# Optimization experiments

Hardware: AMD Instinct MI355X
Metric: run time of the kernel (lower is better)

Reference implementation:

```python
import jax, jax.numpy as jnp
import numpy as np

B, N, E, D, L, NC = 64, 128, 1024, 256, 2, 7
BETA = 0.3  # args.diffloss
BIG = 1e30  # mask_logic constant (score - (1-adj)*1e30), as in torch source lineage


def setup_inputs():
    key = jax.random.key(0)
    ks = iter(jax.random.split(key, 48))
    def p(shape, s=0.02):
        return jax.random.normal(next(ks), shape, jnp.float32) * s
    inp = {}
    inp["features"] = jax.random.normal(next(ks), (B, N, E), jnp.float32)
    inp["adj_1"] = jax.random.randint(next(ks), (B, N, N), 0, 2, jnp.int32)
    inp["adj_2"] = jax.random.randint(next(ks), (B, N, N), 0, 2, jnp.int32)
    inp["s_mask"] = jax.random.randint(next(ks), (B, N, N), 0, 2, jnp.int32)
    inp["s_mask_onehot"] = jnp.zeros((B, N, N, 2), jnp.int32)
    inp["lengths"] = jnp.full((B,), N, jnp.int32)
    inp["fc1_w"] = p((D, E)); inp["fc1_b"] = jnp.zeros((D,), jnp.float32)
    # GRUCell params (torch layout: weight_ih (3D,D) order r,z,n)
    for nm in ["gcs", "gps", "gcl", "gpl"]:
        inp[nm + "_wih"] = p((L, 3 * D, D)); inp[nm + "_whh"] = p((L, 3 * D, D))
        inp[nm + "_bih"] = jnp.zeros((L, 3 * D), jnp.float32)
        inp[nm + "_bhh"] = jnp.zeros((L, 3 * D), jnp.float32)
    # GatDot params per layer: linear1 (Q proj), linear2 (K proj)
    for nm in ["gats", "gatl"]:
        inp[nm + "_wq"] = p((L, D, D)); inp[nm + "_bq"] = jnp.zeros((L, D), jnp.float32)
        inp[nm + "_wk"] = p((L, D, D)); inp[nm + "_bk"] = jnp.zeros((L, D), jnp.float32)
    inp["affine1"] = p((2 * D, 2 * D), 0.05)
    inp["affine2"] = p((2 * D, 2 * D), 0.05)
    IN = 4 * D + E  # hidden*2*2 + emb_dim
    inp["mlp_w1"] = p((D, IN)); inp["mlp_b1"] = jnp.zeros((D,), jnp.float32)
    inp["mlp_w2"] = p((D, D)); inp["mlp_b2"] = jnp.zeros((D,), jnp.float32)
    inp["out_w"] = p((NC, D)); inp["out_b"] = jnp.zeros((NC,), jnp.float32)
    return inp


def gru_cell(x, h, wih, whh, bih, bhh):
    gi = x @ wih.T + bih
    gh = h @ whh.T + bhh
    ir, iz, in_ = jnp.split(gi, 3, axis=-1)
    hr, hz, hn = jnp.split(gh, 3, axis=-1)
    r = jax.nn.sigmoid(ir + hr)
    z = jax.nn.sigmoid(iz + hz)
    n = jnp.tanh(in_ + r * hn)
    return (1.0 - z) * n + z * h


def dag_pass(H_in, adj, gat, cpar, ppar):
    """Sequential DAG pass: per-utterance masked dot-product gather + GRU-C/GRU-P."""
    wq, bq, wk, bk = gat
    n = H_in.shape[1]
    idx = jnp.arange(n)

    def step(carry, inp):
        H1, Kb = carry            # H1: [B,N,D] written prefix; Kb = linear2(H1)
        i, x, arow = inp          # x: [B,D], arow: [B,N]
        q = x @ wq.T + bq
        scores = jnp.einsum('bnd,bd->bn', Kb, q)
        # torch: alpha - (1-adj)*1e30 over prefix :i; positions >= i excluded
        logits = scores - (1.0 - arow) * BIG - (idx >= i).astype(scores.dtype) * (2.0 * BIG)
        w = jax.nn.softmax(logits, axis=-1)
        M = jnp.einsum('bn,bnd->bd', w, H1)  # exactly 0 at i==0 (buffer zeros)
        C = gru_cell(x, M, *cpar)   # grus_c(input=x, hidden=M)
        P = gru_cell(M, x, *ppar)   # grus_p(input=M, hidden=x)
        h = C + P
        H1 = jax.lax.dynamic_update_slice(H1, h[:, None, :], (0, i, 0))
        Kb = jax.lax.dynamic_update_slice(Kb, (h @ wk.T + bk)[:, None, :], (0, i, 0))
        return (H1, Kb), None

    init = (jnp.zeros_like(H_in), jnp.zeros_like(H_in))
    xs = (idx, jnp.swapaxes(H_in, 0, 1), jnp.swapaxes(adj, 0, 1))
    (H1, _), _ = jax.lax.scan(step, init, xs)
    return H1


def diff_loss_fn(a, b):
    # orthogonality (DSN-style) loss between short/long channel features
    x = a.reshape(-1, a.shape[-1])
    y = b.reshape(-1, b.shape[-1])
    x = x - x.mean(axis=0, keepdims=True)
    y = y - y.mean(axis=0, keepdims=True)
    x = x / (jnp.linalg.norm(x, axis=1, keepdims=True) + 1e-6)
    y = y / (jnp.linalg.norm(y, axis=1, keepdims=True) + 1e-6)
    return jnp.mean((x.T @ y) ** 2)


def _forward(features, adj_1, adj_2,
             fc1_w, fc1_b,
             gcs_wih, gcs_whh, gcs_bih, gcs_bhh,
             gps_wih, gps_whh, gps_bih, gps_bhh,
             gcl_wih, gcl_whh, gcl_bih, gcl_bhh,
             gpl_wih, gpl_whh, gpl_bih, gpl_bhh,
             gats_wq, gats_bq, gats_wk, gats_bk,
             gatl_wq, gatl_bq, gatl_wk, gatl_bk,
             affine1, affine2,
             mlp_w1, mlp_b1, mlp_w2, mlp_b2, out_w, out_b):
    adj1 = adj_1.astype(jnp.float32)
    adj2 = adj_2.astype(jnp.float32)
    H0 = jax.nn.relu(features @ fc1_w.T + fc1_b)
    H0r = jax.nn.relu(features[:, ::-1] @ fc1_w.T + fc1_b)
    adj1r = adj1[:, ::-1, ::-1]
    adj2r = adj2[:, ::-1, ::-1]

    def channel(adjf, adjb, wq, bq, wk, bk, cwih, cwhh, cbih, cbhh, pwih, pwhh, pbih, pbhh):
        Hf, Hb = H0, H0r
        outs = []
        for l in range(L):
            gat = (wq[l], bq[l], wk[l], bk[l])
            cp = (cwih[l], cwhh[l], cbih[l], cbhh[l])
            pp = (pwih[l], pwhh[l], pbih[l], pbhh[l])
            Hf = dag_pass(Hf, adjf, gat, cp, pp)
            Hb = dag_pass(Hb, adjb, gat, cp, pp)
            outs.append(jnp.concatenate([Hf, Hb], axis=-1))  # no flip-back (as in source)
        return outs

    cs = channel(adj1, adj1r, gats_wq, gats_bq, gats_wk, gats_bk,
                 gcs_wih, gcs_whh, gcs_bih, gcs_bhh, gps_wih, gps_whh, gps_bih, gps_bhh)
    cl = channel(adj2, adj2r, gatl_wq, gatl_bq, gatl_wk, gatl_bk,
                 gcl_wih, gcl_whh, gcl_bih, gcl_bhh, gpl_wih, gpl_whh, gpl_bih, gpl_bhh)

    dloss = sum(diff_loss_fn(a, b) for a, b in zip(cs, cl)) * BETA

    HS, HL = cs[-1], cl[-1]  # [B,N,2D]
    A1 = jax.nn.softmax(jnp.einsum('bnd,de,bme->bnm', HS, affine1, HL), axis=-1)
    A2 = jax.nn.softmax(jnp.einsum('bnd,de,bme->bnm', HL, affine2, HS), axis=-1)
    HSn = jnp.einsum('bnm,bmd->bnd', A1, HL)
    HLn = jnp.einsum('bnm,bmd->bnd', A2, HS)

    Hfin = jnp.concatenate([features, HSn, HLn], axis=-1)  # in_dim = emb + 4D
    h = jax.nn.relu(Hfin @ mlp_w1.T + mlp_b1)
    h = jax.nn.relu(h @ mlp_w2.T + mlp_b2)
    logits = h @ out_w.T + out_b
    return logits, dloss


def reference(features, adj_1, adj_2, s_mask, s_mask_onehot, lengths,
              fc1_w, fc1_b,
              gcs_wih, gcs_whh, gcs_bih, gcs_bhh,
              gps_wih, gps_whh, gps_bih, gps_bhh,
              gcl_wih, gcl_whh, gcl_bih, gcl_bhh,
              gpl_wih, gpl_whh, gpl_bih, gpl_bhh,
              gats_wq, gats_bq, gats_wk, gats_bk,
              gatl_wq, gatl_bq, gatl_wk, gatl_bk,
              affine1, affine2,
              mlp_w1, mlp_b1, mlp_w2, mlp_b2, out_w, out_b):
    # s_mask / s_mask_onehot / lengths unused for attn_type='dotprod', no_rel_attn=True, nodal_att_type=None
    return _forward(features, adj_1, adj_2,
                    fc1_w, fc1_b,
                    gcs_wih, gcs_whh, gcs_bih, gcs_bhh,
                    gps_wih, gps_whh, gps_bih, gps_bhh,
                    gcl_wih, gcl_whh, gcl_bih, gcl_bhh,
                    gpl_wih, gpl_whh, gpl_bih, gpl_bhh,
                    gats_wq, gats_bq, gats_wk, gats_bk,
                    gatl_wq, gatl_bq, gatl_wk, gatl_bk,
                    affine1, affine2,
                    mlp_w1, mlp_b1, mlp_w2, mlp_b2, out_w, out_b)
```

## Files before the change

### kernel.cpp

```cpp
#include <hip/hip_runtime.h>
#include <hip/hip_fp16.h>
#include <math.h>

#define SB   64
#define SN   128
#define SE   1024
#define SD   256
#define SD2  512
#define SD3  768
#define SIN  2048
#define SNC  7
#define SBN  8192
#define CS   16

#define L_HS   0
#define L_GK   65536
#define L_XH   114688
#define L_QH   122880
#define L_ADJ  131072
#define L_MH   139264
#define L_LG   139776
#define L_WGT  140288
#define L_S0   140800
#define SMEM_BYTES 140864

typedef _Float16 h2v __attribute__((ext_vector_type(2)));

__device__ __forceinline__ float wsum(float v){
#pragma unroll
  for (int o = 32; o; o >>= 1) v += __shfl_xor(v, o);
  return v;
}
__device__ __forceinline__ float sigm(float x){ return 1.f/(1.f + expf(-x)); }

__device__ __forceinline__ unsigned short f2h(float f){
  return __half_as_ushort(__float2half_rn(f));
}
__device__ __forceinline__ float h2f_(unsigned short u){
  return __half2float(__ushort_as_half(u));
}
__device__ __forceinline__ h2v u2h(unsigned u){
  union { unsigned u; h2v h; } c; c.u = u; return c.h;
}
__device__ __forceinline__ float dot8d(uint4 w, uint4 m, float acc){
  acc = __builtin_amdgcn_fdot2(u2h(w.x), u2h(m.x), acc, false);
  acc = __builtin_amdgcn_fdot2(u2h(w.y), u2h(m.y), acc, false);
  acc = __builtin_amdgcn_fdot2(u2h(w.z), u2h(m.z), acc, false);
  acc = __builtin_amdgcn_fdot2(u2h(w.w), u2h(m.w), acc, false);
  return acc;
}

template<bool BKMAJ, bool BIAS, bool RELU, bool ACC>
__global__ __launch_bounds__(256)
void gemm_k(const float* __restrict__ A, const float* __restrict__ Bm,
            const float* __restrict__ bias, float* __restrict__ C,
            int Nn, int K, int lda, int ldb, int ldc,
            long sA, long sB, long sC)
{
  __shared__ float As[16][132];
  __shared__ float Bs[16][68];
  const int t  = threadIdx.x;
  const int tx = t & 15, ty = t >> 4;
  const float* Ab = A + (long)blockIdx.z * sA;
  const float* Bb = Bm + (long)blockIdx.z * sB;
  float* Cb = C + (long)blockIdx.z * sC;
  const int m0 = blockIdx.y * 128, n0 = blockIdx.x * 64;
  float acc[8][4];
#pragma unroll
  for (int i = 0; i < 8; ++i)
#pragma unroll
    for (int j = 0; j < 4; ++j) acc[i][j] = 0.f;

  const int am = t >> 1, ak = (t & 1) * 8;
  int bn_ = 0, bk_ = 0;
  if (BKMAJ) { bk_ = t >> 4; bn_ = (t & 15) * 4; }
  else       { bn_ = t >> 2; bk_ = (t & 3) * 4; }

  for (int k0 = 0; k0 < K; k0 += 16) {
    const float4 a0 = *(const float4*)(Ab + (long)(m0 + am) * lda + k0 + ak);
    const float4 a1 = *(const float4*)(Ab + (long)(m0 + am) * lda + k0 + ak + 4);
    float4 b0;
    if (BKMAJ) b0 = *(const float4*)(Bb + (long)(k0 + bk_) * ldb + n0 + bn_);
    else       b0 = *(const float4*)(Bb + (long)(n0 + bn_) * ldb + k0 + bk_);
    __syncthreads();
    As[ak+0][am] = a0.x; As[ak+1][am] = a0.y; As[ak+2][am] = a0.z; As[ak+3][am] = a0.w;
    As[ak+4][am] = a1.x; As[ak+5][am] = a1.y; As[ak+6][am] = a1.z; As[ak+7][am] = a1.w;
    if (BKMAJ) { *(float4*)&Bs[bk_][bn_] = b0; }
    else { Bs[bk_+0][bn_] = b0.x; Bs[bk_+1][bn_] = b0.y; Bs[bk_+2][bn_] = b0.z; Bs[bk_+3][bn_] = b0.w; }
    __syncthreads();
#pragma unroll
    for (int kk = 0; kk < 16; ++kk) {
      float av[8], bv[4];
      *(float4*)&av[0] = *(const float4*)&As[kk][ty*8];
      *(float4*)&av[4] = *(const float4*)&As[kk][ty*8+4];
      *(float4*)&bv[0] = *(const float4*)&Bs[kk][tx*4];
#pragma unroll
      for (int ii = 0; ii < 8; ++ii)
#pragma unroll
        for (int jj = 0; jj < 4; ++jj)
          acc[ii][jj] = fmaf(av[ii], bv[jj], acc[ii][jj]);
    }
  }
#pragma unroll
  for (int ii = 0; ii < 8; ++ii) {
#pragma unroll
    for (int jj = 0; jj < 4; ++jj) {
      float v = acc[ii][jj];
      if (BIAS) v += bias[n0 + tx*4 + jj];
      const long ci = (long)(m0 + ty*8 + ii) * ldc + n0 + tx*4 + jj;
      if (ACC) v += Cb[ci];
      if (RELU) v = fmaxf(v, 0.f);
      Cb[ci] = v;
    }
  }
}

__global__ void spread_k(const float* __restrict__ src, float* __restrict__ xf,
                         float* __restrict__ xr)
{
  const int r = blockIdx.x, t = threadIdx.x;
  const int b = r >> 7, n = r & 127;
  const float v = src[(long)r * SD + t];
  xf[((long)(n * 64 + b)) * SD + t] = v;
  xr[((long)((127 - n) * 64 + b)) * SD + t] = v;
}

struct PTArgs { const float* wc[4]; const float* wp[4]; unsigned short* Wt; };
__global__ void packT_k(PTArgs a)
{
  const int kb8 = blockIdx.x, cd = blockIdx.y, t = threadIdx.x;
#pragma unroll
  for (int p = 0; p < 6; ++p) {
    const int r = t + 256 * p;
    const float* src = (r < 768) ? (a.wc[cd] + (long)r * SD)
                                 : (a.wp[cd] + (long)(r - 768) * SD);
    const float4 v0 = *(const float4*)(src + kb8 * 8);
    const float4 v1 = *(const float4*)(src + kb8 * 8 + 4);
    uint4 o;
    o.x = (unsigned)f2h(v0.x) | ((unsigned)f2h(v0.y) << 16);
    o.y = (unsigned)f2h(v0.z) | ((unsigned)f2h(v0.w) << 16);
    o.z = (unsigned)f2h(v1.x) | ((unsigned)f2h(v1.y) << 16);
    o.w = (unsigned)f2h(v1.z) | ((unsigned)f2h(v1.w) << 16);
    *(uint4*)(a.Wt + (((size_t)cd * 32 + kb8) * 1536 + r) * 8) = o;
  }
}

__global__ void s0_k(const float* __restrict__ Q, const float* __restrict__ bk,
                     float* __restrict__ S0)
{
  const int r = blockIdx.x * 4 + (threadIdx.x >> 6), lane = threadIdx.x & 63;
  const float4 q  = *(const float4*)(Q + (long)r * SD + lane * 4);
  const float4 kb = *(const float4*)(bk + lane * 4);
  float p = q.x*kb.x + q.y*kb.y + q.z*kb.z + q.w*kb.w;
  p = wsum(p);
  if (lane == 0) S0[r] = p;
}

struct StepArgs {
  const float* Qt[4]; const float* S0[4];
  const int* adj[4]; int rev[4];
  const float* bc[4];  const float* bp[4];
  const float* bgc[4]; const float* bgp[4];
  const float* X[4];
  float* H1[4];
  const unsigned short* Wt;
  const unsigned short* Wgk;
  int ldX;
};
__global__ __launch_bounds__(256, 1) void step_layer_k(StepArgs a)
{
  extern __shared__ __align__(16) char dsm[];
  unsigned short* Hs  = (unsigned short*)(dsm + L_HS);
  unsigned short* GKh = (unsigned short*)(dsm + L_GK);
  unsigned short* Xh  = (unsigned short*)(dsm + L_XH);
  unsigned short* Qh  = (unsigned short*)(dsm + L_QH);
  float* adjc = (float*)(dsm + L_ADJ);
  unsigned short* Mh  = (unsigned short*)(dsm + L_MH);
  float* lg   = (float*)(dsm + L_LG);
  float* wgt  = (float*)(dsm + L_WGT);
  float* s0s  = (float*)(dsm + L_S0);

  const int blk = blockIdx.x;
  const int cd = blk & 3, b = blk >> 2;
  const int t = threadIdx.x, j = t;
  const int ldX = a.ldX;
  const float* Xp  = a.X[cd];
  float* H1 = a.H1[cd];
  const float* Qtp = a.Qt[cd];
  const float* S0p = a.S0[cd];
  const int*   adjp = a.adj[cd];
  const int    rev  = a.rev[cd];

  const float bc0 = a.bc[cd][j],  bc1 = a.bc[cd][256+j],  bc2 = a.bc[cd][512+j];
  const float bp0 = a.bp[cd][j],  bp1 = a.bp[cd][256+j],  bp2 = a.bp[cd][512+j];
  const unsigned short* wb   = a.Wt  + ((size_t)cd*32*1536 + j)*8;
  const unsigned short* wbgk = a.Wgk + ((size_t)cd*32*1536 + j)*8;

  for (int c0 = 0; c0 < SN; c0 += CS) {
    __syncthreads();
#pragma unroll
    for (int s = 0; s < CS; ++s) {
      Xh[s*256 + t] = f2h(Xp[((long)(c0+s)*64 + b)*ldX + t]);
      Qh[s*256 + t] = f2h(Qtp[((long)(c0+s)*64 + b)*SD + t]);
    }
    for (int z = t; z < CS*128; z += 256) {
      const int s = z >> 7, n = z & 127;
      const int i = c0 + s;
      int av = 0;
      if (i > 0) {
        const int ii = rev ? (SN-1-i) : i;
        const int nn = rev ? (SN-1-n) : n;
        av = adjp[((long)b*SN + ii)*SN + nn];
      }
      adjc[z] = (float)av;
    }
    if (t < CS) s0s[t] = S0p[(c0+t)*64 + b];
    __syncthreads();

    {
      float gacc[6][CS];
#pragma unroll
      for (int g = 0; g < 6; ++g)
#pragma unroll
        for (int s = 0; s < CS; ++s) gacc[g][s] = 0.f;
      uint4 wA[6], wB[6];
#pragma unroll
      for (int g = 0; g < 6; ++g) {
        wA[g] = ((const uint4*)wbgk)[g*256];
        wB[g] = ((const uint4*)(wbgk + 12288))[g*256];
      }
      for (int kb8 = 0; kb8 < 32; kb8 += 2) {
#pragma unroll
        for (int s = 0; s < CS; ++s) {
          const uint4 x8 = *(const uint4*)&Xh[s*256 + kb8*8];
#pragma unroll
          for (int g = 0; g < 6; ++g) gacc[g][s] = dot8d(wA[g], x8, gacc[g][s]);
        }
        if (kb8 + 2 < 32) {
          const uint4* wr = (const uint4*)(wbgk + (size_t)(kb8+2)*12288);
#pragma unroll
          for (int g = 0; g < 6; ++g) wA[g] = wr[g*256];
        }
#pragma unroll
        for (int s = 0; s < CS; ++s) {
          const uint4 x8 = *(const uint4*)&Xh[s*256 + kb8*8 + 8];
#pragma unroll
          for (int g = 0; g < 6; ++g) gacc[g][s] = dot8d(wB[g], x8, gacc[g][s]);
        }
        if (kb8 + 3 < 32) {
          const uint4* wr = (const uint4*)(wbgk + (size_t)(kb8+3)*12288);
#pragma unroll
          for (int g = 0; g < 6; ++g) wB[g] = wr[g*256];
        }
      }
#pragma unroll
      for (int g = 0; g < 6; ++g) {
        const float bg = (g < 3) ? a.bgc[cd][g*256 + j] : a.bgp[cd][(g-3)*256 + j];
#pragma unroll
        for (int s = 0; s < CS; ++s)
          GKh[s*1536 + g*256 + j] = f2h(gacc[g][s] + bg);
      }
    }
    __syncthreads();

    for (int s = 0; s < CS; ++s) {
      const int i = c0 + s;
      const float xj = Xp[((long)i*64 + b)*ldX + j];
      uint4 wA[6], wB[6], wC[6], wD[6];
#pragma unroll
      for (int g = 0; g < 6; ++g) {
        wA[g] = ((const uint4*)wb)[g*256];
        wB[g] = ((const uint4*)(wb + 12288))[g*256];
        wC[g] = ((const uint4*)(wb + 24576))[g*256];
        wD[g] = ((const uint4*)(wb + 36864))[g*256];
      }
      float mreg;
      if (i == 0) {
        Mh[t] = 0;
        mreg = 0.f;
        __syncthreads();
      } else {
        if (t < 128 && (t & 64) < i) {
          const int n = t;
          const char* hrow = (const char*)Hs + n*512;
          const int cx = (n & 31) << 4;
          const unsigned short* qrow = Qh + s*256;
          float acc = 0.f;
#pragma unroll
          for (int k = 0; k < 32; ++k) {
            const uint4 hv = *(const uint4*)(hrow + ((k*16) ^ cx));
            const uint4 qv = *(const uint4*)(qrow + k*8);
            acc = dot8d(hv, qv, acc);
          }
          lg[n] = acc;
        }
        __syncthreads();
        if (t < 64) {
          const float s0v = s0s[s];
          const int l = t;
          const float v0 = (l < i)    ? (lg[l]    + s0v - (1.f - adjc[s*128+l]   )*1e30f) : -3.0e38f;
          const float v1 = (l+64 < i) ? (lg[l+64] + s0v - (1.f - adjc[s*128+l+64])*1e30f) : -3.0e38f;
          float mx = fmaxf(v0, v1);
#pragma unroll
          for (int o = 32; o; o >>= 1) mx = fmaxf(mx, __shfl_xor(mx, o));
          const float e0 = (l < i)    ? expf(v0 - mx) : 0.f;
          const float e1 = (l+64 < i) ? expf(v1 - mx) : 0.f;
          float sum = e0 + e1;
#pragma unroll
          for (int o = 32; o; o >>= 1) sum += __shfl_xor(sum, o);
          const float inv = 1.f / sum;
          if (l < i)    wgt[l]    = e0 * inv;
          if (l+64 < i) wgt[l+64] = e1 * inv;
        }
        __syncthreads();
        float m0 = 0.f, m1 = 0.f, m2 = 0.f, m3 = 0.f;
        int n = 0;
        for (; n + 4 <= i; n += 4) {
          m0 = fmaf(wgt[n+0], h2f_(Hs[(n+0)*256 + (j ^ (((n+0)&31)<<3))]), m0);
          m1 = fmaf(wgt[n+1], h2f_(Hs[(n+1)*256 + (j ^ (((n+1)&31)<<3))]), m1);
          m2 = fmaf(wgt[n+2], h2f_(Hs[(n+2)*256 + (j ^ (((n+2)&31)<<3))]), m2);
          m3 = fmaf(wgt[n+3], h2f_(Hs[(n+3)*256 + (j ^ (((n+3)&31)<<3))]), m3);
        }
        for (; n < i; ++n)
          m0 = fmaf(wgt[n], h2f_(Hs[n*256 + (j ^ ((n&31)<<3))]), m0);
        mreg = (m0 + m1) + (m2 + m3);
        Mh[t] = f2h(mreg);
        __syncthreads();
      }

      float g0 = 0.f, g1 = 0.f, g2 = 0.f, g3 = 0.f, g4 = 0.f, g5 = 0.f;
      for (int kb = 0; kb < 32; kb += 4) {
        {
          const uint4 m8 = *(const uint4*)&Mh[kb*8];
          g0 = dot8d(wA[0], m8, g0); g1 = dot8d(wA[1], m8, g1);
          g2 = dot8d(wA[2], m8, g2); g3 = dot8d(wA[3], m8, g3);
          g4 = dot8d(wA[4], m8, g4); g5 = dot8d(wA[5], m8, g5);
        }
        if (kb < 28) {
          const uint4* w = (const uint4*)(wb + (size_t)(kb+4)*12288);
#pragma unroll
          for (int g = 0; g < 6; ++g) wA[g] = w[g*256];
        }
        {
          const uint4 m8 = *(const uint4*)&Mh[kb*8 + 8];
          g0 = dot8d(wB[0], m8, g0); g1 = dot8d(wB[1], m8, g1);
          g2 = dot8d(wB[2], m8, g2); g3 = dot8d(wB[3], m8, g3);
          g4 = dot8d(wB[4], m8, g4); g5 = dot8d(wB[5], m8, g5);
        }
        if (kb < 28) {
          const uint4* w = (const uint4*)(wb + (size_t)(kb+5)*12288);
#pragma unroll
          for (int g = 0; g < 6; ++g) wB[g] = w[g*256];
        }
        {
          const uint4 m8 = *(const uint4*)&Mh[kb*8 + 16];
          g0 = dot8d(wC[0], m8, g0); g1 = dot8d(wC[1], m8, g1);
          g2 = dot8d(wC[2], m8, g2); g3 = dot8d(wC[3], m8, g3);
          g4 = dot8d(wC[4], m8, g4); g5 = dot8d(wC[5], m8, g5);
        }
        if (kb < 28) {
          const uint4* w = (const uint4*)(wb + (size_t)(kb+6)*12288);
#pragma unroll
          for (int g = 0; g < 6; ++g) wC[g] = w[g*256];
        }
        {
          const uint4 m8 = *(const uint4*)&Mh[kb*8 + 24];
          g0 = dot8d(wD[0], m8, g0); g1 = dot8d(wD[1], m8, g1);
          g2 = dot8d(wD[2], m8, g2); g3 = dot8d(wD[3], m8, g3);
          g4 = dot8d(wD[4], m8, g4); g5 = dot8d(wD[5], m8, g5);
        }
        if (kb < 28) {
          const uint4* w = (const uint4*)(wb + (size_t)(kb+7)*12288);
#pragma unroll
          for (int g = 0; g < 6; ++g) wD[g] = w[g*256];
        }
      }

      {
        const int sb = s*1536;
        const float gic_r = h2f_(GKh[sb + j]);
        const float gic_z = h2f_(GKh[sb + 256 + j]);
        const float gic_n = h2f_(GKh[sb + 512 + j]);
        const float ghp_r = h2f_(GKh[sb + 768 + j]);
        const float ghp_z = h2f_(GKh[sb + 1024 + j]);
        const float ghp_n = h2f_(GKh[sb + 1280 + j]);
        const float rC = sigm(gic_r + g0 + bc0);
        const float zC = sigm(gic_z + g1 + bc1);
        const float nC = tanhf(gic_n + rC * (g2 + bc2));
        const float Cc = (1.f - zC) * nC + zC * mreg;
        const float rP = sigm(g3 + bp0 + ghp_r);
        const float zP = sigm(g4 + bp1 + ghp_z);
        const float nP = tanhf(g5 + bp2 + rP * ghp_n);
        const float hval = Cc + (1.f - zP) * nP + zP * xj;
        H1[((long)i*64 + b)*SD2 + j] = hval;
        Hs[i*256 + (j ^ ((i & 31) << 3))] = f2h(hval);
      }
      __syncthreads();
    }
  }
}

__global__ void zero_k(float* p, long n)
{
  for (long idx = (long)blockIdx.x * 256 + threadIdx.x; idx < n; idx += (long)gridDim.x * 256)
    p[idx] = 0.f;
}

__global__ void colmean_k(const float* __restrict__ X, float* __restrict__ mean)
{
  __shared__ float red[256];
  const int c = blockIdx.x * 64 + (threadIdx.x & 63), rq = threadIdx.x >> 6;
  const int r0 = blockIdx.y * 256;
  float acc = 0.f;
  for (int r = r0 + rq; r < r0 + 256; r += 4) acc += X[(long)r * SD2 + c];
  red[threadIdx.x] = acc;
  __syncthreads();
  if (threadIdx.x < 64) {
    const float s = red[threadIdx.x] + red[64 + threadIdx.x] + red[128 + threadIdx.x] + red[192 + threadIdx.x];
    atomicAdd(&mean[c], s * (1.f / 8192.f));
  }
}

__global__ void rownorm_k(const float* __restrict__ X, const float* __restrict__ mean,
                          float* __restrict__ inv)
{
  const int r = blockIdx.x * 4 + (threadIdx.x >> 6), lane = threadIdx.x & 63;
  const float* xp = X + (long)r * SD2 + lane * 8;
  const float4 v0 = *(const float4*)xp;
  const float4 v1 = *(const float4*)(xp + 4);
  const float4 m0 = *(const float4*)(mean + lane * 8);
  const float4 m1 = *(const float4*)(mean + lane * 8 + 4);
  float ss = 0.f, d;
  d = v0.x - m0.x; ss += d*d;  d = v0.y - m0.y; ss += d*d;
  d = v0.z - m0.z; ss += d*d;  d = v0.w - m0.w; ss += d*d;
  d = v1.x - m1.x; ss += d*d;  d = v1.y - m1.y; ss += d*d;
  d = v1.z - m1.z; ss += d*d;  d = v1.w - m1.w; ss += d*d;
  ss = wsum(ss);
  if (lane == 0) inv[r] = 1.f / (sqrtf(ss) + 1e-6f);
}

__global__ __launch_bounds__(256)
void gpart_k(const float* __restrict__ X, const float* __restrict__ Y,
             const float* __restrict__ mx, const float* __restrict__ my,
             const float* __restrict__ ix, const float* __restrict__ iy,
             float* __restrict__ G)
{
  __shared__ float As[16][68];
  __shared__ float Bs[16][68];
  __shared__ float mxs[64], mys[64];
  const int t = threadIdx.x, tx = t & 15, ty = t >> 4;
  const int ci = blockIdx.y * 64, cj = blockIdx.x * 64;
  if (t < 64) { mxs[t] = mx[ci + t]; mys[t] = my[cj + t]; }
  float acc[4][4];
#pragma unroll
  for (int ii = 0; ii < 4; ++ii)
#pragma unroll
    for (int jj = 0; jj < 4; ++jj) acc[ii][jj] = 0.f;
  const int rl = t >> 4, c4 = (t & 15) * 4;
  __syncthreads();
  const int kend = blockIdx.z * 512 + 512;
  for (int kb = blockIdx.z * 512; kb < kend; kb += 16) {
    const int r = kb + rl;
    const float4 xv = *(const float4*)(X + (long)r * SD2 + ci + c4);
    const float4 yv = *(const float4*)(Y + (long)r * SD2 + cj + c4);
    const float vx = ix[r], vy = iy[r];
    __syncthreads();
    As[rl][c4+0] = (xv.x - mxs[c4+0]) * vx; As[rl][c4+1] = (xv.y - mxs[c4+1]) * vx;
    As[rl][c4+2] = (xv.z - mxs[c4+2]) * vx; As[rl][c4+3] = (xv.w - mxs[c4+3]) * vx;
    Bs[rl][c4+0] = (yv.x - mys[c4+0]) * vy; Bs[rl][c4+1] = (yv.y - mys[c4+1]) * vy;
    Bs[rl][c4+2] = (yv.z - mys[c4+2]) * vy; Bs[rl][c4+3] = (yv.w - mys[c4+3]) * vy;
    __syncthreads();
#pragma unroll
    for (int kk = 0; kk < 16; ++kk) {
      float av[4], bv[4];
      *(float4*)&av[0] = *(const float4*)&As[kk][ty*4];
      *(float4*)&bv[0] = *(const float4*)&Bs[kk][tx*4];
#pragma unroll
      for (int ii = 0; ii < 4; ++ii)
#pragma unroll
        for (int jj = 0; jj < 4; ++jj)
          acc[ii][jj] = fmaf(av[ii], bv[jj], acc[ii][jj]);
    }
  }
#pragma unroll
  for (int ii = 0; ii < 4; ++ii)
#pragma unroll
    for (int jj = 0; jj < 4; ++jj)
      atomicAdd(&G[(long)(ci + ty*4 + ii) * SD2 + cj + tx*4 + jj], acc[ii][jj]);
}

__global__ void sqsum_k(const float* __restrict__ G, float* __restrict__ dl)
{
  __shared__ float red[4];
  float s = 0.f;
  const long base = (long)blockIdx.x * 1024;
#pragma unroll
  for (int it = 0; it < 4; ++it) { const float v = G[base + it*256 + threadIdx.x]; s += v*v; }
  s = wsum(s);
  const int lane = threadIdx.x & 63, wv = threadIdx.x >> 6;
  if (lane == 0) red[wv] = s;
  __syncthreads();
  if (threadIdx.x == 0) atomicAdd(dl, red[0] + red[1] + red[2] + red[3]);
}

__global__ void smax_k(float* __restrict__ S)
{
  const int r = blockIdx.x * 4 + (threadIdx.x >> 6), lane = threadIdx.x & 63;
  float* p = S + (long)r * SN;
  const float v0 = p[lane], v1 = p[lane + 64];
  float mx = fmaxf(v0, v1);
#pragma unroll
  for (int o = 32; o; o >>= 1) mx = fmaxf(mx, __shfl_xor(mx, o));
  const float e0 = expf(v0 - mx), e1 = expf(v1 - mx);
  float s = e0 + e1;
#pragma unroll
  for (int o = 32; o; o >>= 1) s += __shfl_xor(s, o);
  const float inv = 1.f / s;
  p[lane] = e0 * inv; p[lane + 64] = e1 * inv;
}

__global__ void head_k(const float* __restrict__ H, const float* __restrict__ W,
                       const float* __restrict__ bo, float* __restrict__ out)
{
  const int r = blockIdx.x * 4 + (threadIdx.x >> 6), lane = threadIdx.x & 63;
  const float4 h = *(const float4*)(H + (long)r * SD + lane * 4);
#pragma unroll
  for (int c = 0; c < SNC; ++c) {
    const float4 w = *(const float4*)(W + (long)c * SD + lane * 4);
    float p = h.x*w.x + h.y*w.y + h.z*w.z + h.w*w.w;
    p = wsum(p);
    if (lane == 0) out[(long)r * SNC + c] = p + bo[c];
  }
}

__global__ void fin_k(const float* __restrict__ dl, float* __restrict__ out)
{
  out[0] = (dl[0] + dl[1]) * (0.3f / (512.f * 512.f));
}

extern "C" void kernel_launch(void* const* d_in, const int* in_sizes, int n_in,
                              void* d_out, int out_size, void* d_ws, size_t ws_size,
                              hipStream_t stream)
{
  (void)in_sizes; (void)n_in; (void)out_size; (void)ws_size;

  static bool attr_set = false;
  if (!attr_set) {
    hipFuncSetAttribute(reinterpret_cast<const void*>(step_layer_k),
                        hipFuncAttributeMaxDynamicSharedMemorySize, SMEM_BYTES);
    attr_set = true;
  }

  const float* F    = (const float*)d_in[0];
  const int*   adj1 = (const int*)  d_in[1];
  const int*   adj2 = (const int*)  d_in[2];
  const float* fc1w = (const float*)d_in[6];
  const float* fc1b = (const float*)d_in[7];
  const float *g_wih[4], *g_whh[4], *g_bih[4], *g_bhh[4];
  for (int g = 0; g < 4; ++g) {
    g_wih[g] = (const float*)d_in[8 + g*4 + 0];
    g_whh[g] = (const float*)d_in[8 + g*4 + 1];
    g_bih[g] = (const float*)d_in[8 + g*4 + 2];
    g_bhh[g] = (const float*)d_in[8 + g*4 + 3];
  }
  const float* gat_wq[2] = {(const float*)d_in[24], (const float*)d_in[28]};
  const float* gat_bq[2] = {(const float*)d_in[25], (const float*)d_in[29]};
  const float* gat_wk[2] = {(const float*)d_in[26], (const float*)d_in[30]};
  const float* gat_bk[2] = {(const float*)d_in[27], (const float*)d_in[31]};
  const float* aff1 = (const float*)d_in[32];
  const float* aff2 = (const float*)d_in[33];
  const float* mw1  = (const float*)d_in[34];
  const float* mb1  = (const float*)d_in[35];
  const float* mw2  = (const float*)d_in[36];
  const float* mb2  = (const float*)d_in[37];
  const float* ow   = (const float*)d_in[38];
  const float* ob   = (const float*)d_in[39];
  float* out = (float*)d_out;

  float* ws = (float*)d_ws;
  size_t off = 0;
  auto take = [&](size_t nf){ float* p = ws + off; off += nf; return p; };
  float* region = take(22552576);
  float* X0f  = region;
  float* X0r  = region + 2097152;
  float* Qtb  = region + 4194304;
  float* Qtmp = region + 12582912;
  float* Htmp = region + 14680064;
  float* T  = region;
  float* Sb = region + 4194304;
  float* HH = region + 5242880;
  float* h1 = region + 9437184;
  float* h2 = region + 11534336;
  float* Ocat[2][2];
  for (int c = 0; c < 2; ++c) for (int l = 0; l < 2; ++l) Ocat[c][l] = take(4194304);
  float* S0b   = take(32768);
  unsigned short* WtB  = (unsigned short*)take(786432);
  unsigned short* WgkB = (unsigned short*)take(786432);
  float* meanx = take(512);
  float* meany = take(512);
  float* invx  = take(8192);
  float* invy  = take(8192);
  float* dl    = take(8);
  float* Gbuf  = take(262144);

  gemm_k<false,true,true,false><<<dim3(4,64,1),256,0,stream>>>(
      F, fc1w, fc1b, Htmp, SD, SE, SE, SE, SD, 0,0,0);
  spread_k<<<SBN,256,0,stream>>>(Htmp, X0f, X0r);

  for (int l = 0; l < 2; ++l) {
    PTArgs pt, pg; StepArgs sta;
    sta.ldX = l ? SD2 : SD;
    sta.Wt = WtB; sta.Wgk = WgkB;
    const int ldX = sta.ldX;
    for (int cd = 0; cd < 4; ++cd) {
      const int ch = cd >> 1;
      const float* X = (l == 0) ? ((cd & 1) ? X0r : X0f)
                                : (Ocat[ch][0] + (cd & 1) * SD);
      const float* wq   = gat_wq[ch] + l * SD * SD;
      const float* bq   = gat_bq[ch] + l * SD;
      const float* wk   = gat_wk[ch] + l * SD * SD;
      const float* bk   = gat_bk[ch] + l * SD;
      const float* cwih = g_wih[ch*2+0] + l * SD3 * SD;
      const float* cwhh = g_whh[ch*2+0] + l * SD3 * SD;
      const float* cbih = g_bih[ch*2+0] + l * SD3;
      const float* cbhh = g_bhh[ch*2+0] + l * SD3;
      const float* pwih = g_wih[ch*2+1] + l * SD3 * SD;
      const float* pwhh = g_whh[ch*2+1] + l * SD3 * SD;
      const float* pbih = g_bih[ch*2+1] + l * SD3;
      const float* pbhh = g_bhh[ch*2+1] + l * SD3;
      pt.wc[cd] = cwhh; pt.wp[cd] = pwih;
      pg.wc[cd] = cwih; pg.wp[cd] = pwhh;
      gemm_k<false,true,false,false><<<dim3(4,64,1),256,0,stream>>>(
          X, wq, bq, Qtmp, SD, SD, ldX, SD, SD, 0,0,0);
      gemm_k<true,false,false,false><<<dim3(4,64,1),256,0,stream>>>(
          Qtmp, wk, nullptr, Qtb + (size_t)cd*2097152, SD, SD, SD, SD, SD, 0,0,0);
      s0_k<<<SBN/4,256,0,stream>>>(Qtmp, bk, S0b + cd*SBN);
      float* H1mut = Ocat[ch][l] + (cd & 1) * SD;
      sta.Qt[cd] = Qtb + (size_t)cd*2097152;
      sta.S0[cd] = S0b + cd*SBN;
      sta.H1[cd] = H1mut;
      sta.adj[cd] = ch ? adj2 : adj1; sta.rev[cd] = cd & 1;
      sta.bc[cd]  = cbhh; sta.bp[cd]  = pbih;
      sta.bgc[cd] = cbih; sta.bgp[cd] = pbhh;
      sta.X[cd] = X;
    }
    pt.Wt = WtB;  packT_k<<<dim3(32,4),256,0,stream>>>(pt);
    pg.Wt = WgkB; packT_k<<<dim3(32,4),256,0,stream>>>(pg);

    step_layer_k<<<256,256,SMEM_BYTES,stream>>>(sta);
  }

  zero_k<<<1,256,0,stream>>>(dl, 2);
  for (int l = 0; l < 2; ++l) {
    zero_k<<<4,256,0,stream>>>(meanx, 1024);
    colmean_k<<<dim3(8,32,1),256,0,stream>>>(Ocat[0][l], meanx);
    colmean_k<<<dim3(8,32,1),256,0,stream>>>(Ocat[1][l], meany);
    rownorm_k<<<SBN/4,256,0,stream>>>(Ocat[0][l], meanx, invx);
    rownorm_k<<<SBN/4,256,0,stream>>>(Ocat[1][l], meany, invy);
    zero_k<<<256,256,0,stream>>>(Gbuf, (long)SD2*SD2);
    gpart_k<<<dim3(8,8,16),256,0,stream>>>(Ocat[0][l], Ocat[1][l], meanx, meany, invx, invy, Gbuf);
    sqsum_k<<<256,256,0,stream>>>(Gbuf, dl + l);
  }

  gemm_k<true,false,false,false><<<dim3(8,64,1),256,0,stream>>>(
      Ocat[0][1], aff1, nullptr, T, SD2, SD2, SD2, SD2, SD2, 0,0,0);
  gemm_k<false,false,false,false><<<dim3(2,1,64),256,0,stream>>>(
      T, Ocat[1][1], nullptr, Sb, SN, SD2, 64*SD2, 64*SD2, SN, SD2, SD2, (long)SN*SN);
  smax_k<<<SBN/4,256,0,stream>>>(Sb);
  gemm_k<true,false,false,false><<<dim3(8,1,64),256,0,stream>>>(
      Sb, Ocat[1][1], nullptr, HH, SD2, SN, SN, 64*SD2, SD2, (long)SN*SN, SD2, (long)SN*SD2);
  gemm_k<false,true,false,false><<<dim3(4,64,1),256,0,stream>>>(
      F, mw1, mb1, h1, SD, SE, SE, SIN, SD, 0,0,0);
  gemm_k<false,false,false,true><<<dim3(4,64,1),256,0,stream>>>(
      HH, mw1 + 1024, nullptr, h1, SD, SD2, SD2, SIN, SD, 0,0,0);
  gemm_k<true,false,false,false><<<dim3(8,64,1),256,0,stream>>>(
      Ocat[1][1], aff2, nullptr, T, SD2, SD2, SD2, SD2, SD2, 0,0,0);
  gemm_k<false,false,false,false><<<dim3(2,1,64),256,0,stream>>>(
      T, Ocat[0][1], nullptr, Sb, SN, SD2, 64*SD2, 64*SD2, SN, SD2, SD2, (long)SN*SN);
  smax_k<<<SBN/4,256,0,stream>>>(Sb);
  gemm_k<true,false,false,false><<<dim3(8,1,64),256,0,stream>>>(
      Sb, Ocat[0][1], nullptr, HH, SD2, SN, SN, 64*SD2, SD2, (long)SN*SN, SD2, (long)SN*SD2);
  gemm_k<false,false,true,true><<<dim3(4,64,1),256,0,stream>>>(
      HH, mw1 + 1536, nullptr, h1, SD, SD2, SD2, SIN, SD, 0,0,0);
  gemm_k<false,true,true,false><<<dim3(4,64,1),256,0,stream>>>(
      h1, mw2, mb2, h2, SD, SD, SD, SD, SD, 0,0,0);
  head_k<<<SBN/4,256,0,stream>>>(h2, ow, ob, out);
  fin_k<<<1,1,0,stream>>>(dl, out + SBN * SNC);
}
```

Baseline: 5.586 ms.

## Split GRU-C and GRU-P gate work across two 256-thread halves in step kernel

The sequential DAG step kernel now launches 512 threads per block. One half computes the GRU-C gates and the other the GRU-P gates, so per-thread weight registers and dot products drop from six gate rows to three. The attention logit dot product is also split across 256 threads into two partial sums. The P result is exchanged through a small shared buffer, which adds extra barriers inside divergent branches and doubles register pressure per block. The aim is to shorten the latency-bound per-utterance critical path.

```diff
diff --git a/kernel.cpp b/kernel.cpp
--- a/kernel.cpp
+++ b/kernel.cpp
@@ -19,10 +19,11 @@
 #define L_QH   122880
 #define L_ADJ  131072
 #define L_MH   139264
-#define L_LG   139776
-#define L_WGT  140288
-#define L_S0   140800
-#define SMEM_BYTES 140864
+#define L_LGP  139776
+#define L_WGT  140800
+#define L_PBUF 141312
+#define L_S0   142336
+#define SMEM_BYTES 142400
 
 typedef _Float16 h2v __attribute__((ext_vector_type(2)));
 
@@ -167,7 +168,7 @@
   const unsigned short* Wgk;
   int ldX;
 };
-__global__ __launch_bounds__(256, 1) void step_layer_k(StepArgs a)
+__global__ __launch_bounds__(512, 2) void step_layer_k(StepArgs a)
 {
   extern __shared__ __align__(16) char dsm[];
   unsigned short* Hs  = (unsigned short*)(dsm + L_HS);
@@ -176,13 +177,15 @@
   unsigned short* Qh  = (unsigned short*)(dsm + L_QH);
   float* adjc = (float*)(dsm + L_ADJ);
   unsigned short* Mh  = (unsigned short*)(dsm + L_MH);
-  float* lg   = (float*)(dsm + L_LG);
+  float* lgp  = (float*)(dsm + L_LGP);
   float* wgt  = (float*)(dsm + L_WGT);
+  float* pbuf = (float*)(dsm + L_PBUF);
   float* s0s  = (float*)(dsm + L_S0);
 
   const int blk = blockIdx.x;
   const int cd = blk & 3, b = blk >> 2;
-  const int t = threadIdx.x, j = t;
+  const int t = threadIdx.x;
+  const int half = t >> 8, j = t & 255;
   const int ldX = a.ldX;
   const float* Xp  = a.X[cd];
   float* H1 = a.H1[cd];
@@ -191,19 +194,24 @@
   const int*   adjp = a.adj[cd];
   const int    rev  = a.rev[cd];
 
-  const float bc0 = a.bc[cd][j],  bc1 = a.bc[cd][256+j],  bc2 = a.bc[cd][512+j];
-  const float bp0 = a.bp[cd][j],  bp1 = a.bp[cd][256+j],  bp2 = a.bp[cd][512+j];
-  const unsigned short* wb   = a.Wt  + ((size_t)cd*32*1536 + j)*8;
-  const unsigned short* wbgk = a.Wgk + ((size_t)cd*32*1536 + j)*8;
+  float eb0, eb1, eb2, gb0, gb1, gb2;
+  if (half == 0) {
+    eb0 = a.bc[cd][j];  eb1 = a.bc[cd][256+j];  eb2 = a.bc[cd][512+j];
+    gb0 = a.bgc[cd][j]; gb1 = a.bgc[cd][256+j]; gb2 = a.bgc[cd][512+j];
+  } else {
+    eb0 = a.bp[cd][j];  eb1 = a.bp[cd][256+j];  eb2 = a.bp[cd][512+j];
+    gb0 = a.bgp[cd][j]; gb1 = a.bgp[cd][256+j]; gb2 = a.bgp[cd][512+j];
+  }
+  const unsigned short* wb   = a.Wt  + ((size_t)cd*32*1536 + half*768 + j)*8;
+  const unsigned short* wbgk = a.Wgk + ((size_t)cd*32*1536 + half*768 + j)*8;
 
   for (int c0 = 0; c0 < SN; c0 += CS) {
-    __syncthreads();
-#pragma unroll
-    for (int s = 0; s < CS; ++s) {
-      Xh[s*256 + t] = f2h(Xp[((long)(c0+s)*64 + b)*ldX + t]);
-      Qh[s*256 + t] = f2h(Qtp[((long)(c0+s)*64 + b)*SD + t]);
-    }
-    for (int z = t; z < CS*128; z += 256) {
+    for (int z = t; z < CS*256; z += 512) {
+      const int s = z >> 8, c = z & 255;
+      Xh[z] = f2h(Xp[((long)(c0+s)*64 + b)*ldX + c]);
+      Qh[z] = f2h(Qtp[((long)(c0+s)*64 + b)*SD + c]);
+    }
+    for (int z = t; z < CS*128; z += 512) {
       const int s = z >> 7, n = z & 127;
       const int i = c0 + s;
       int av = 0;
@@ -218,14 +226,14 @@
     __syncthreads();
 
     {
-      float gacc[6][CS];
-#pragma unroll
-      for (int g = 0; g < 6; ++g)
+      float gacc[3][CS];
+#pragma unroll
+      for (int g = 0; g < 3; ++g)
 #pragma unroll
         for (int s = 0; s < CS; ++s) gacc[g][s] = 0.f;
-      uint4 wA[6], wB[6];
-#pragma unroll
-      for (int g = 0; g < 6; ++g) {
+      uint4 wA[3], wB[3];
+#pragma unroll
+      for (int g = 0; g < 3; ++g) {
         wA[g] = ((const uint4*)wbgk)[g*256];
         wB[g] = ((const uint4*)(wbgk + 12288))[g*256];
       }
@@ -234,72 +242,72 @@
         for (int s = 0; s < CS; ++s) {
           const uint4 x8 = *(const uint4*)&Xh[s*256 + kb8*8];
 #pragma unroll
-          for (int g = 0; g < 6; ++g) gacc[g][s] = dot8d(wA[g], x8, gacc[g][s]);
+          for (int g = 0; g < 3; ++g) gacc[g][s] = dot8d(wA[g], x8, gacc[g][s]);
         }
         if (kb8 + 2 < 32) {
           const uint4* wr = (const uint4*)(wbgk + (size_t)(kb8+2)*12288);
 #pragma unroll
-          for (int g = 0; g < 6; ++g) wA[g] = wr[g*256];
+          for (int g = 0; g < 3; ++g) wA[g] = wr[g*256];
         }
 #pragma unroll
         for (int s = 0; s < CS; ++s) {
           const uint4 x8 = *(const uint4*)&Xh[s*256 + kb8*8 + 8];
 #pragma unroll
-          for (int g = 0; g < 6; ++g) gacc[g][s] = dot8d(wB[g], x8, gacc[g][s]);
+          for (int g = 0; g < 3; ++g) gacc[g][s] = dot8d(wB[g], x8, gacc[g][s]);
         }
         if (kb8 + 3 < 32) {
           const uint4* wr = (const uint4*)(wbgk + (size_t)(kb8+3)*12288);
 #pragma unroll
-          for (int g = 0; g < 6; ++g) wB[g] = wr[g*256];
+          for (int g = 0; g < 3; ++g) wB[g] = wr[g*256];
         }
       }
-#pragma unroll
-      for (int g = 0; g < 6; ++g) {
-        const float bg = (g < 3) ? a.bgc[cd][g*256 + j] : a.bgp[cd][(g-3)*256 + j];
+      const float gb[3] = {gb0, gb1, gb2};
+#pragma unroll
+      for (int g = 0; g < 3; ++g)
 #pragma unroll
         for (int s = 0; s < CS; ++s)
-          GKh[s*1536 + g*256 + j] = f2h(gacc[g][s] + bg);
-      }
+          GKh[s*1536 + (half*3+g)*256 + j] = f2h(gacc[g][s] + gb[g]);
     }
     __syncthreads();
 
     for (int s = 0; s < CS; ++s) {
       const int i = c0 + s;
       const float xj = Xp[((long)i*64 + b)*ldX + j];
-      uint4 wA[6], wB[6], wC[6], wD[6];
-#pragma unroll
-      for (int g = 0; g < 6; ++g) {
+      uint4 wA[3], wB[3], wC[3], wD[3];
+#pragma unroll
+      for (int g = 0; g < 3; ++g) {
         wA[g] = ((const uint4*)wb)[g*256];
         wB[g] = ((const uint4*)(wb + 12288))[g*256];
         wC[g] = ((const uint4*)(wb + 24576))[g*256];
         wD[g] = ((const uint4*)(wb + 36864))[g*256];
       }
-      float mreg;
+      float mreg = 0.f;
       if (i == 0) {
-        Mh[t] = 0;
-        mreg = 0.f;
+        if (t < 256) Mh[t] = 0;
         __syncthreads();
       } else {
-        if (t < 128 && (t & 64) < i) {
-          const int n = t;
+        if (t < 256) {
+          const int n = t & 127, hi = t >> 7;
           const char* hrow = (const char*)Hs + n*512;
           const int cx = (n & 31) << 4;
-          const unsigned short* qrow = Qh + s*256;
+          const unsigned short* qrow = Qh + s*256 + hi*128;
           float acc = 0.f;
 #pragma unroll
-          for (int k = 0; k < 32; ++k) {
-            const uint4 hv = *(const uint4*)(hrow + ((k*16) ^ cx));
+          for (int k = 0; k < 16; ++k) {
+            const uint4 hv = *(const uint4*)(hrow + ((((hi*16 + k)*16)) ^ cx));
             const uint4 qv = *(const uint4*)(qrow + k*8);
             acc = dot8d(hv, qv, acc);
           }
-          lg[n] = acc;
+          lgp[t] = acc;
         }
         __syncthreads();
         if (t < 64) {
           const float s0v = s0s[s];
           const int l = t;
-          const float v0 = (l < i)    ? (lg[l]    + s0v - (1.f - adjc[s*128+l]   )*1e30f) : -3.0e38f;
-          const float v1 = (l+64 < i) ? (lg[l+64] + s0v - (1.f - adjc[s*128+l+64])*1e30f) : -3.0e38f;
+          const float lg0 = lgp[l]      + lgp[128 + l];
+          const float lg1 = lgp[64 + l] + lgp[192 + l];
+          const float v0 = (l < i)    ? (lg0 + s0v - (1.f - adjc[s*128+l]   )*1e30f) : -3.0e38f;
+          const float v1 = (l+64 < i) ? (lg1 + s0v - (1.f - adjc[s*128+l+64])*1e30f) : -3.0e38f;
           float mx = fmaxf(v0, v1);
 #pragma unroll
           for (int o = 32; o; o >>= 1) mx = fmaxf(mx, __shfl_xor(mx, o));
@@ -313,89 +321,83 @@
           if (l+64 < i) wgt[l+64] = e1 * inv;
         }
         __syncthreads();
-        float m0 = 0.f, m1 = 0.f, m2 = 0.f, m3 = 0.f;
-        int n = 0;
-        for (; n + 4 <= i; n += 4) {
-          m0 = fmaf(wgt[n+0], h2f_(Hs[(n+0)*256 + (j ^ (((n+0)&31)<<3))]), m0);
-          m1 = fmaf(wgt[n+1], h2f_(Hs[(n+1)*256 + (j ^ (((n+1)&31)<<3))]), m1);
-          m2 = fmaf(wgt[n+2], h2f_(Hs[(n+2)*256 + (j ^ (((n+2)&31)<<3))]), m2);
-          m3 = fmaf(wgt[n+3], h2f_(Hs[(n+3)*256 + (j ^ (((n+3)&31)<<3))]), m3);
-        }
-        for (; n < i; ++n)
-          m0 = fmaf(wgt[n], h2f_(Hs[n*256 + (j ^ ((n&31)<<3))]), m0);
-        mreg = (m0 + m1) + (m2 + m3);
-        Mh[t] = f2h(mreg);
+        if (half == 0) {
+          float m0 = 0.f, m1 = 0.f, m2 = 0.f, m3 = 0.f;
+          int n = 0;
+          for (; n + 4 <= i; n += 4) {
+            m0 = fmaf(wgt[n+0], h2f_(Hs[(n+0)*256 + (j ^ (((n+0)&31)<<3))]), m0);
+            m1 = fmaf(wgt[n+1], h2f_(Hs[(n+1)*256 + (j ^ (((n+1)&31)<<3))]), m1);
+            m2 = fmaf(wgt[n+2], h2f_(Hs[(n+2)*256 + (j ^ (((n+2)&31)<<3))]), m2);
+            m3 = fmaf(wgt[n+3], h2f_(Hs[(n+3)*256 + (j ^ (((n+3)&31)<<3))]), m3);
+          }
+          for (; n < i; ++n)
+            m0 = fmaf(wgt[n], h2f_(Hs[n*256 + (j ^ ((n&31)<<3))]), m0);
+          mreg = (m0 + m1) + (m2 + m3);
+          Mh[j] = f2h(mreg);
+        }
         __syncthreads();
       }
 
-      float g0 = 0.f, g1 = 0.f, g2 = 0.f, g3 = 0.f, g4 = 0.f, g5 = 0.f;
+      float g0 = 0.f, g1 = 0.f, g2 = 0.f;
       for (int kb = 0; kb < 32; kb += 4) {
         {
           const uint4 m8 = *(const uint4*)&Mh[kb*8];
-          g0 = dot8d(wA[0], m8, g0); g1 = dot8d(wA[1], m8, g1);
-          g2 = dot8d(wA[2], m8, g2); g3 = dot8d(wA[3], m8, g3);
-          g4 = dot8d(wA[4], m8, g4); g5 = dot8d(wA[5], m8, g5);
+          g0 = dot8d(wA[0], m8, g0); g1 = dot8d(wA[1], m8, g1); g2 = dot8d(wA[2], m8, g2);
         }
         if (kb < 28) {
           const uint4* w = (const uint4*)(wb + (size_t)(kb+4)*12288);
-#pragma unroll
-          for (int g = 0; g < 6; ++g) wA[g] = w[g*256];
+          wA[0] = w[0]; wA[1] = w[256]; wA[2] = w[512];
         }
         {
           const uint4 m8 = *(const uint4*)&Mh[kb*8 + 8];
-          g0 = dot8d(wB[0], m8, g0); g1 = dot8d(wB[1], m8, g1);
-          g2 = dot8d(wB[2], m8, g2); g3 = dot8d(wB[3], m8, g3);
-          g4 = dot8d(wB[4], m8, g4); g5 = dot8d(wB[5], m8, g5);
+          g0 = dot8d(wB[0], m8, g0); g1 = dot8d(wB[1], m8, g1); g2 = dot8d(wB[2], m8, g2);
         }
         if (kb < 28) {
           const uint4* w = (const uint4*)(wb + (size_t)(kb+5)*12288);
-#pragma unroll
-          for (int g = 0; g < 6; ++g) wB[g] = w[g*256];
+          wB[0] = w[0]; wB[1] = w[256]; wB[2] = w[512];
         }
         {
           const uint4 m8 = *(const uint4*)&Mh[kb*8 + 16];
-          g0 = dot8d(wC[0], m8, g0); g1 = dot8d(wC[1], m8, g1);
-          g2 = dot8d(wC[2], m8, g2); g3 = dot8d(wC[3], m8, g3);
-          g4 = dot8d(wC[4], m8, g4); g5 = dot8d(wC[5], m8, g5);
+          g0 = dot8d(wC[0], m8, g0); g1 = dot8d(wC[1], m8, g1); g2 = dot8d(wC[2], m8, g2);
         }
         if (kb < 28) {
           const uint4* w = (const uint4*)(wb + (size_t)(kb+6)*12288);
-#pragma unroll
-          for (int g = 0; g < 6; ++g) wC[g] = w[g*256];
+          wC[0] = w[0]; wC[1] = w[256]; wC[2] = w[512];
         }
         {
           const uint4 m8 = *(const uint4*)&Mh[kb*8 + 24];
-          g0 = dot8d(wD[0], m8, g0); g1 = dot8d(wD[1], m8, g1);
-          g2 = dot8d(wD[2], m8, g2); g3 = dot8d(wD[3], m8, g3);
-          g4 = dot8d(wD[4], m8, g4); g5 = dot8d(wD[5], m8, g5);
+          g0 = dot8d(wD[0], m8, g0); g1 = dot8d(wD[1], m8, g1); g2 = dot8d(wD[2], m8, g2);
         }
         if (kb < 28) {
           const uint4* w = (const uint4*)(wb + (size_t)(kb+7)*12288);
-#pragma unroll
-          for (int g = 0; g < 6; ++g) wD[g] = w[g*256];
+          wD[0] = w[0]; wD[1] = w[256]; wD[2] = w[512];
         }
       }
 
       {
-        const int sb = s*1536;
-        const float gic_r = h2f_(GKh[sb + j]);
-        const float gic_z = h2f_(GKh[sb + 256 + j]);
-        const float gic_n = h2f_(GKh[sb + 512 + j]);
-        const float ghp_r = h2f_(GKh[sb + 768 + j]);
-        const float ghp_z = h2f_(GKh[sb + 1024 + j]);
-        const float ghp_n = h2f_(GKh[sb + 1280 + j]);
-        const float rC = sigm(gic_r + g0 + bc0);
-        const float zC = sigm(gic_z + g1 + bc1);
-        const float nC = tanhf(gic_n + rC * (g2 + bc2));
-        const float Cc = (1.f - zC) * nC + zC * mreg;
-        const float rP = sigm(g3 + bp0 + ghp_r);
-        const float zP = sigm(g4 + bp1 + ghp_z);
-        const float nP = tanhf(g5 + bp2 + rP * ghp_n);
-        const float hval = Cc + (1.f - zP) * nP + zP * xj;
-        H1[((long)i*64 + b)*SD2 + j] = hval;
-        Hs[i*256 + (j ^ ((i & 31) << 3))] = f2h(hval);
+        const int sb = s*1536 + half*768;
+        const float gk0 = h2f_(GKh[sb + j]);
+        const float gk1 = h2f_(GKh[sb + 256 + j]);
+        const float gk2 = h2f_(GKh[sb + 512 + j]);
+        if (half == 1) {
+          const float rP = sigm(g0 + eb0 + gk0);
+          const float zP = sigm(g1 + eb1 + gk1);
+          const float nP = tanhf(g2 + eb2 + rP * gk2);
+          pbuf[j] = (1.f - zP) * nP + zP * xj;
+          __syncthreads();
+          __syncthreads();
+        } else {
+          const float rC = sigm(gk0 + g0 + eb0);
+          const float zC = sigm(gk1 + g1 + eb1);
+          const float nC = tanhf(gk2 + rC * (g2 + eb2));
+          const float Cc = (1.f - zC) * nC + zC * mreg;
+          __syncthreads();
+          const float hval = Cc + pbuf[j];
+          H1[((long)i*64 + b)*SD2 + j] = hval;
+          Hs[i*256 + (j ^ ((i & 31) << 3))] = f2h(hval);
+          __syncthreads();
+        }
       }
-      __syncthreads();
     }
   }
 }
@@ -647,7 +649,7 @@
     pt.Wt = WtB;  packT_k<<<dim3(32,4),256,0,stream>>>(pt);
     pg.Wt = WgkB; packT_k<<<dim3(32,4),256,0,stream>>>(pg);
 
-    step_layer_k<<<256,256,SMEM_BYTES,stream>>>(sta);
+    step_layer_k<<<256,512,SMEM_BYTES,stream>>>(sta);
   }
 
   zero_k<<<1,256,0,stream>>>(dl, 2);
```

Result: slower. 8.599 ms (+53.9%).
